# Optimization experiments

Measured on AMD Instinct MI355X. Metric: run time of the kernel, lower is better.

The kernel has to match this reference:

```python
import jax, jax.numpy as jnp
import numpy as np

H, D, VD = 8, 64, 64
QD, KD, VDIM, OUT = 512, 512, 512, 512
N, QS, VS = 16, 512, 512
TEMP = 10.0              # softstair_temp
SCALING = D ** -0.5


def _softstair(x):
    fl = jnp.floor(x)
    return fl + jax.nn.sigmoid(TEMP * (jnp.abs(x - fl) - 0.5))


def setup_inputs() -> dict:
    key = jax.random.key(0)
    ks = jax.random.split(key, 24)
    f = jax.random.normal
    s = 0.03  # xavier-ish scale
    return {
        "Q": f(ks[0], (N, QS, QD), jnp.float32),
        "K": f(ks[1], (N, VS, KD), jnp.float32),
        "V": f(ks[2], (N, VS, VDIM), jnp.float32),
        "past_state": f(ks[3], (N, H, QS, D), jnp.float32),
        "past_attention": jax.random.uniform(ks[4], (N, H, QS, 1), jnp.float32),
        "value_positions": jnp.arange(VS, dtype=jnp.float32),
        "attention_mask": jnp.ones((N, QS, VS), jnp.int32),
        "Wq": f(ks[5], (QD, H * D), jnp.float32) * s,
        "Wk": f(ks[6], (KD, H * D), jnp.float32) * s,
        "Wv": f(ks[7], (VDIM, H * VD), jnp.float32) * s,
        "Wpos": f(ks[8], (QD, H * D), jnp.float32) * s,
        "bpos": f(ks[9], (H * D,), jnp.float32) * s,
        "Wsigma": f(ks[10], (H, D, 1), jnp.float32) * s,
        "Wrho": f(ks[11], (H, D, 3), jnp.float32) * s,
        "mix_w": f(ks[12], (QD, 1), jnp.float32) * s,
        "mix_b": f(ks[13], (1,), jnp.float32) * s,
        "gru_wi": f(ks[14], (D, 3 * D), jnp.float32) * s,
        "gru_wh": f(ks[15], (D, 3 * D), jnp.float32) * s,
        "gru_bi": f(ks[16], (3 * D,), jnp.float32) * s,
        "gru_bh": f(ks[17], (3 * D,), jnp.float32) * s,
        "Wc": f(ks[18], (H * VD, OUT), jnp.float32) * s,
    }


def reference(Q, K, V, past_state, past_attention, value_positions, attention_mask,
              Wq, Wk, Wv, Wpos, bpos, Wsigma, Wrho, mix_w, mix_b,
              gru_wi, gru_wh, gru_bi, gru_bh, Wc):
    n, qS, _ = Q.shape
    vS = K.shape[1]
    mask_f = attention_mask.astype(jnp.float32)          # [N,qS,vS]
    mask_b = attention_mask.astype(bool)[:, None]        # [N,1,qS,vS]
    lengths = jnp.sum(mask_f, axis=-1)                   # [N,qS]
    l_1 = jnp.maximum(1.0, lengths - 1.0)[:, None, :, None]
    step_size = 1.0 / l_1                                # [N,1,qS,1]
    nvp = value_positions[None, None, None, :] * step_size  # [N,1,qS,vS]

    # mix gate
    mix = jax.nn.sigmoid(Q @ mix_w + mix_b)[:, None]     # [N,1,qS,1]

    # projections -> [N,H,S,d]
    Qpos = (Q @ Wpos + bpos).reshape(n, qS, H, D).transpose(0, 2, 1, 3)
    Qh = (Q @ Wq).reshape(n, qS, H, D).transpose(0, 2, 1, 3)
    Kh = (K @ Wk).reshape(n, vS, H, D).transpose(0, 2, 1, 3)
    Vh = (V @ Wv).reshape(n, vS, H, VD).transpose(0, 2, 1, 3)

    # content attention
    content = jnp.einsum('bhqd,bhkd->bhqk', Qh, Kh) * SCALING
    content_attn = jax.nn.softmax(jnp.where(mask_b, content, -jnp.inf), axis=-1)

    # GRUCell update (torch gate order r,z,n) on relu(Qpos) with past_state
    x = jax.nn.relu(Qpos)
    gi = x @ gru_wi + gru_bi
    gh = past_state @ gru_wh + gru_bh
    ir, iz, inn = jnp.split(gi, 3, axis=-1)
    hr, hz, hn = jnp.split(gh, 3, axis=-1)
    r = jax.nn.sigmoid(ir + hr)
    z = jax.nn.sigmoid(iz + hz)
    nn_ = jnp.tanh(inn + r * hn)
    state = (1.0 - z) * nn_ + z * past_state             # [N,H,qS,D]

    # location (Gaussian) attention
    sigma = (jax.nn.relu(jnp.einsum('bhqd,hde->bhqe', state, Wsigma)) + 0.27) \
            / lengths[:, None, :, None]                  # [N,H,qS,1]
    rho = jnp.einsum('bhqd,hde->bhqe', state, Wrho)      # [N,H,qS,3]
    steps = _softstair(rho[..., 0:1])
    attn_gate = jax.nn.sigmoid(rho[..., 1:2])
    bias_gate = jax.nn.sigmoid(rho[..., 2:3])
    mu_ = steps * step_size + attn_gate * past_attention + bias_gate
    # leaky clamp to [0,1]
    mu = jnp.maximum(0.01 * mu_, jnp.minimum(mu_, 1.0 + 0.01 * mu_))
    diff = nvp - mu                                      # [N,H,qS,vS]
    gauss = jnp.exp(-(diff * diff) / (2.0 * sigma * sigma))
    g = gauss * mask_f[:, None]
    pos_attn = g / jnp.sum(g + 1e-20, axis=-1, keepdims=True)

    scores = mix * pos_attn + (1.0 - mix) * content_attn
    attended = jnp.einsum('bhqk,bhkv->bhqv', scores, Vh)
    out = attended.transpose(0, 2, 1, 3).reshape(n, qS, H * VD) @ Wc
    return out
```

## Files before the change

kernel.cpp:

```cpp
#include <hip/hip_runtime.h>


typedef __bf16 bf16;
typedef __bf16 bfx8 __attribute__((ext_vector_type(8)));
typedef float v4f __attribute__((ext_vector_type(4)));

__device__ inline float sigm(float x) { return 1.0f / (1.0f + __expf(-x)); }
__device__ inline float tanh_fast(float x) { return 1.0f - 2.0f / (__expf(2.0f * x) + 1.0f); }

__device__ inline v4f mfma16(bfx8 a, bfx8 b, v4f c) {
    return __builtin_amdgcn_mfma_f32_16x16x32_bf16(a, b, c, 0, 0, 0);
}

typedef const __attribute__((address_space(1))) void* gvp;
typedef __attribute__((address_space(3))) void* lvp;

__device__ inline void gload_lds16(const bf16* g, bf16* l) {
    __builtin_amdgcn_global_load_lds((gvp)g, (lvp)l, 16, 0, 0);
}

__device__ inline void split8(const float* __restrict__ p, bfx8& hi, bfx8& lo) {
    float4 x = *(const float4*)p;
    float4 y = *(const float4*)(p + 4);
    float v[8] = {x.x, x.y, x.z, x.w, y.x, y.y, y.z, y.w};
#pragma unroll
    for (int j = 0; j < 8; ++j) {
        bf16 h = (bf16)v[j];
        hi[j] = h;
        lo[j] = (bf16)(v[j] - (float)h);
    }
}

struct TW { const float* src[5]; bf16* dst[5]; bf16* dstlo[5]; };

__global__ __launch_bounds__(256) void trans_w_kernel(TW a) {
    __shared__ float tile[64][68];
    const float* src = a.src[blockIdx.y];
    bf16* dst = a.dst[blockIdx.y];
    bf16* dlo = a.dstlo[blockIdx.y];
    const int rbase = (blockIdx.x >> 3) * 64, cbase = (blockIdx.x & 7) * 64;
    const int t = threadIdx.x;
    const int r = t >> 2, cc = (t & 3) * 16;
    {
        const float* p = src + (long)(rbase + r) * 512 + cbase + cc;
        *(float4*)(&tile[r][cc]) = *(const float4*)p;
        *(float4*)(&tile[r][cc + 4]) = *(const float4*)(p + 4);
        *(float4*)(&tile[r][cc + 8]) = *(const float4*)(p + 8);
        *(float4*)(&tile[r][cc + 12]) = *(const float4*)(p + 12);
    }
    __syncthreads();
    {
        bfx8 h0, h1, l0, l1;
#pragma unroll
        for (int j = 0; j < 8; ++j) {
            float v0 = tile[cc + j][r];
            float v1 = tile[cc + 8 + j][r];
            bf16 a0 = (bf16)v0, a1 = (bf16)v1;
            h0[j] = a0; l0[j] = (bf16)(v0 - (float)a0);
            h1[j] = a1; l1[j] = (bf16)(v1 - (float)a1);
        }
        const int n_ = cbase + r;
        const int x_ = (n_ & 7) << 3;
        const long rowo = (long)n_ * 512;
        const int ka = (rbase + cc) ^ x_;
        const int kb = (rbase + cc + 8) ^ x_;
        *(bfx8*)(dst + rowo + ka) = h0;
        *(bfx8*)(dst + rowo + kb) = h1;
        if (dlo) {
            *(bfx8*)(dlo + rowo + ka) = l0;
            *(bfx8*)(dlo + rowo + kb) = l1;
        }
    }
}

__global__ void gru_prep_kernel(const float* __restrict__ gwi, const float* __restrict__ gwh,
                                bf16* ih, bf16* il, bf16* hh, bf16* hl) {
    const float* src = blockIdx.x ? gwh : gwi;
    bf16* dh = blockIdx.x ? hh : ih;
    bf16* dl = blockIdx.x ? hl : il;
    int n = threadIdx.x;
    for (int k = 0; k < 64; ++k) {
        float v = src[k * 192 + n];
        bf16 h = (bf16)v;
        dh[n * 64 + k] = h;
        dl[n * 64 + k] = (bf16)(v - (float)h);
    }
}

struct GEMMDesc {
    const float* Af;
    const bf16* Ab;
    const bf16* B0;
    const bf16* B1;
    const float* bias;
    bf16* Cb;
    bf16* Cl;
    float* Cf;
    int mode;
};
struct G4 { GEMMDesc d[4]; };

__global__ __launch_bounds__(256, 4) void gemm128(G4 gg) {
    __shared__ bf16 sm[16384];
    bf16* As = sm;
    bf16* Bs = sm + 8192;

    const GEMMDesc g = gg.d[blockIdx.z];
    const int mode = g.mode;
    const int mbase = blockIdx.x * 128, nbase = blockIdx.y * 128;
    const int t = threadIdx.x, w = t >> 6, l = t & 63;
    const int quad = l >> 4, c = l & 15;
    const int wr = w >> 1, wc = w & 1;

    const v4f zero4 = {0.f, 0.f, 0.f, 0.f};
    v4f acc[4][4];
#pragma unroll
    for (int m = 0; m < 4; ++m)
#pragma unroll
        for (int nn = 0; nn < 4; ++nn) acc[m][nn] = zero4;

    const int nsteps = (mode == 2) ? 24 : 8;
    const int arow_t = t >> 3;
    const int ach = t & 7;
    const int asw = ((ach ^ (arow_t & 7)) * 8);
    const int xm = c & 7;

    for (int s = 0; s < nsteps; ++s) {
        const bf16* Bsrc = g.B0;
        int k0;
        bool lo = false;
        if (mode == 2) {
            int ph = s >> 3;
            k0 = (s & 7) * 64;
            if (ph == 1) Bsrc = g.B1;
            lo = (ph == 2);
        } else {
            k0 = s * 64;
        }

#pragma unroll
        for (int j = 0; j < 4; ++j) {
            int slot = w * 4 + j;
            int row = slot * 8 + (l >> 3);
            const bf16* src = Bsrc + (long)(nbase + row) * 512 + k0 + (l & 7) * 8;
            gload_lds16(src, Bs + slot * 512);
        }
        if (mode == 3) {
#pragma unroll
            for (int j = 0; j < 4; ++j) {
                int slot = w * 4 + j;
                int row = slot * 8 + (l >> 3);
                const bf16* src = g.Ab + (long)(mbase + row) * 512 + k0 + (l & 7) * 8;
                gload_lds16(src, As + slot * 512);
            }
        } else {
#pragma unroll
            for (int j = 0; j < 4; ++j) {
                int row = j * 32 + arow_t;
                const float* p = g.Af + (long)(mbase + row) * 512 + k0 + ach * 8;
                float4 x = *(const float4*)p, y = *(const float4*)(p + 4);
                float v[8] = {x.x, x.y, x.z, x.w, y.x, y.y, y.z, y.w};
                bfx8 hv;
                if (!lo) {
#pragma unroll
                    for (int q = 0; q < 8; ++q) hv[q] = (bf16)v[q];
                } else {
#pragma unroll
                    for (int q = 0; q < 8; ++q) {
                        bf16 h = (bf16)v[q];
                        hv[q] = (bf16)(v[q] - (float)h);
                    }
                }
                *(bfx8*)(&As[row * 64 + asw]) = hv;
            }
        }
        __syncthreads();

#pragma unroll
        for (int ks = 0; ks < 2; ++ks) {
            const int off = (((ks * 4 + quad) ^ xm) * 8);
            bfx8 af[4], bb[4];
#pragma unroll
            for (int m = 0; m < 4; ++m)
                af[m] = *(const bfx8*)(&As[(wr * 64 + m * 16 + c) * 64 + off]);
#pragma unroll
            for (int nn = 0; nn < 4; ++nn)
                bb[nn] = *(const bfx8*)(&Bs[(wc * 64 + nn * 16 + c) * 64 + off]);
#pragma unroll
            for (int m = 0; m < 4; ++m)
#pragma unroll
                for (int nn = 0; nn < 4; ++nn)
                    acc[m][nn] = mfma16(af[m], bb[nn], acc[m][nn]);
        }
        __syncthreads();
    }

    if (mode == 3) {
        float* C = g.Cf;
#pragma unroll
        for (int m = 0; m < 4; ++m)
#pragma unroll
            for (int nn = 0; nn < 4; ++nn)
#pragma unroll
                for (int i = 0; i < 4; ++i) {
                    int row = mbase + wr * 64 + m * 16 + quad * 4 + i;
                    int col = nbase + wc * 64 + nn * 16 + c;
                    C[(long)row * 512 + col] = acc[m][nn][i];
                }
        return;
    }

    if (mode == 1) {
        bf16* CT = g.Cb + ((long)(mbase >> 9)) * 262144;
        const int s0 = mbase & 511;
        for (int h = 0; h < 2; ++h) {
            if (wr == h) {
#pragma unroll
                for (int m = 0; m < 4; ++m)
#pragma unroll
                    for (int nn = 0; nn < 4; ++nn)
#pragma unroll
                        for (int i = 0; i < 4; ++i)
                            sm[(wc * 64 + nn * 16 + c) * 64 + m * 16 + quad * 4 + i] =
                                (bf16)acc[m][nn][i];
            }
            __syncthreads();
            {
                const bf16* src = sm + (t >> 1) * 64 + (t & 1) * 32;
                bf16* d = CT + (long)(nbase + (t >> 1)) * 512 + s0 + h * 64 + (t & 1) * 32;
#pragma unroll
                for (int j = 0; j < 4; ++j) *(bfx8*)(d + j * 8) = *(const bfx8*)(src + j * 8);
            }
            __syncthreads();
        }
        return;
    }

    for (int h = 0; h < 2; ++h) {
        if (wr == h) {
#pragma unroll
            for (int m = 0; m < 4; ++m)
#pragma unroll
                for (int nn = 0; nn < 4; ++nn)
#pragma unroll
                    for (int i = 0; i < 4; ++i) {
                        int col = wc * 64 + nn * 16 + c;
                        float v = acc[m][nn][i];
                        if (mode == 2) v = fmaxf(v + g.bias[nbase + col], 0.f);
                        bf16 hv = (bf16)v;
                        sm[(m * 16 + quad * 4 + i) * 128 + col] = hv;
                        if (mode == 2)
                            sm[8192 + (m * 16 + quad * 4 + i) * 128 + col] =
                                (bf16)(v - (float)hv);
                    }
        }
        __syncthreads();
        {
            const int row = t >> 2, seg = t & 3;
            const bf16* src = sm + row * 128 + seg * 32;
            bf16* d = g.Cb + (long)(mbase + h * 64 + row) * 512 + nbase + seg * 32;
#pragma unroll
            for (int j = 0; j < 4; ++j) *(bfx8*)(d + j * 8) = *(const bfx8*)(src + j * 8);
            if (mode == 2) {
                const bf16* src2 = sm + 8192 + row * 128 + seg * 32;
                bf16* d2 = g.Cl + (long)(mbase + h * 64 + row) * 512 + nbase + seg * 32;
#pragma unroll
                for (int j = 0; j < 4; ++j) *(bfx8*)(d2 + j * 8) = *(const bfx8*)(src2 + j * 8);
            }
        }
        __syncthreads();
    }
}

__global__ __launch_bounds__(256) void mix_len_kernel(
    const float* __restrict__ Q, const int* __restrict__ mask,
    const float* __restrict__ mix_w, const float* __restrict__ mix_b,
    float* __restrict__ mixv, float* __restrict__ stepv, float* __restrict__ lenv,
    unsigned* __restrict__ maskbits) {
    int row = blockIdx.x * 4 + (threadIdx.x >> 6);
    int lane = threadIdx.x & 63;
    float dot = 0.f, ms = 0.f;
    unsigned myw = 0;
#pragma unroll
    for (int j = 0; j < 8; ++j) {
        float qv = Q[(long)row * 512 + j * 64 + lane];
        float wv = mix_w[j * 64 + lane];
        dot += qv * wv;
        int mv = mask[(long)row * 512 + j * 64 + lane];
        unsigned long long b = __ballot(mv != 0);
        ms += (float)__popcll(b);
        if ((lane >> 1) == j) myw = (unsigned)(b >> ((lane & 1) * 32));
    }
#pragma unroll
    for (int o = 32; o > 0; o >>= 1) dot += __shfl_xor(dot, o);
    if (lane < 16) maskbits[(long)row * 16 + lane] = myw;
    if (lane == 0) {
        mixv[row] = sigm(dot + mix_b[0]);
        lenv[row] = ms;
        stepv[row] = 1.0f / fmaxf(1.0f, ms - 1.0f);
    }
}

__global__ __launch_bounds__(256) void gru_fused_kernel(
    const bf16* __restrict__ Xh, const bf16* __restrict__ Xl,
    const float* __restrict__ hp,
    const bf16* __restrict__ wih, const bf16* __restrict__ wil,
    const bf16* __restrict__ whh, const bf16* __restrict__ whl,
    const float* __restrict__ gbi, const float* __restrict__ gbh,
    const float* __restrict__ pa, const float* __restrict__ Wsigma,
    const float* __restrict__ Wrho,
    const float* __restrict__ lenv, const float* __restrict__ stepv,
    float* __restrict__ muv, float* __restrict__ sigv) {
    __shared__ bf16 Wh[192][72], Wl[192][72];
    __shared__ float biL[384];

    const int b = blockIdx.x;
    const int qb = b & 7, nh = b >> 3, hd = nh & 7, n = nh >> 3;
    const int t = threadIdx.x;
    const int w = t >> 6, lane = t & 63, quad = lane >> 4, c = lane & 15;
    const int q0 = qb * 64 + w * 16;

    if (t < 192) { biL[t] = gbi[t]; biL[192 + t] = gbh[t]; }
#pragma unroll
    for (int it = 0; it < 6; ++it) {
        int task = it * 256 + t;
        int r = task >> 3, ch = task & 7;
        *(bfx8*)(&Wh[r][ch * 8]) = *(const bfx8*)(wih + r * 64 + ch * 8);
        *(bfx8*)(&Wl[r][ch * 8]) = *(const bfx8*)(wil + r * 64 + ch * 8);
    }
    __syncthreads();

    const v4f zero4 = {0.f, 0.f, 0.f, 0.f};
    v4f gi[12], gh[12];
#pragma unroll
    for (int nt = 0; nt < 12; ++nt) gi[nt] = zero4;
#pragma unroll
    for (int ks = 0; ks < 2; ++ks) {
        long ao = (long)(n * 512 + q0 + c) * 512 + hd * 64 + ks * 32 + quad * 8;
        bfx8 xh = *(const bfx8*)(Xh + ao);
        bfx8 xl = *(const bfx8*)(Xl + ao);
#pragma unroll
        for (int nt = 0; nt < 12; ++nt) {
            bfx8 bh = *(const bfx8*)(&Wh[nt * 16 + c][ks * 32 + quad * 8]);
            bfx8 bl = *(const bfx8*)(&Wl[nt * 16 + c][ks * 32 + quad * 8]);
            gi[nt] = mfma16(xh, bh, gi[nt]);
            gi[nt] = mfma16(xh, bl, gi[nt]);
            gi[nt] = mfma16(xl, bh, gi[nt]);
        }
    }
    __syncthreads();
#pragma unroll
    for (int it = 0; it < 6; ++it) {
        int task = it * 256 + t;
        int r = task >> 3, ch = task & 7;
        *(bfx8*)(&Wh[r][ch * 8]) = *(const bfx8*)(whh + r * 64 + ch * 8);
        *(bfx8*)(&Wl[r][ch * 8]) = *(const bfx8*)(whl + r * 64 + ch * 8);
    }
    __syncthreads();
#pragma unroll
    for (int nt = 0; nt < 12; ++nt) gh[nt] = zero4;
#pragma unroll
    for (int ks = 0; ks < 2; ++ks) {
        bfx8 ah, al;
        split8(hp + (long)(nh * 512 + q0 + c) * 64 + ks * 32 + quad * 8, ah, al);
#pragma unroll
        for (int nt = 0; nt < 12; ++nt) {
            bfx8 bh = *(const bfx8*)(&Wh[nt * 16 + c][ks * 32 + quad * 8]);
            bfx8 bl = *(const bfx8*)(&Wl[nt * 16 + c][ks * 32 + quad * 8]);
            gh[nt] = mfma16(ah, bh, gh[nt]);
            gh[nt] = mfma16(ah, bl, gh[nt]);
            gh[nt] = mfma16(al, bh, gh[nt]);
        }
    }

    float st[4][4];
#pragma unroll
    for (int t4 = 0; t4 < 4; ++t4) {
        float bir = biL[t4 * 16 + c];
        float biz = biL[64 + t4 * 16 + c];
        float bin = biL[128 + t4 * 16 + c];
        float bhr = biL[192 + t4 * 16 + c];
        float bhz = biL[256 + t4 * 16 + c];
        float bhn = biL[320 + t4 * 16 + c];
#pragma unroll
        for (int i = 0; i < 4; ++i) {
            int row = q0 + quad * 4 + i;
            float r = sigm(gi[t4][i] + bir + gh[t4][i] + bhr);
            float z = sigm(gi[t4 + 4][i] + biz + gh[t4 + 4][i] + bhz);
            float nn_ = tanh_fast(gi[t4 + 8][i] + bin + r * (gh[t4 + 8][i] + bhn));
            float hpv = hp[(long)(nh * 512 + row) * 64 + t4 * 16 + c];
            st[t4][i] = (1.0f - z) * nn_ + z * hpv;
        }
    }

    float ws_[4], wr0[4], wr1[4], wr2[4];
#pragma unroll
    for (int t4 = 0; t4 < 4; ++t4) {
        int d = t4 * 16 + c;
        ws_[t4] = Wsigma[hd * 64 + d];
        wr0[t4] = Wrho[(hd * 64 + d) * 3 + 0];
        wr1[t4] = Wrho[(hd * 64 + d) * 3 + 1];
        wr2[t4] = Wrho[(hd * 64 + d) * 3 + 2];
    }
#pragma unroll
    for (int i = 0; i < 4; ++i) {
        float s0 = 0.f, s1 = 0.f, s2 = 0.f, s3 = 0.f;
#pragma unroll
        for (int t4 = 0; t4 < 4; ++t4) {
            float sv = st[t4][i];
            s0 += sv * ws_[t4];
            s1 += sv * wr0[t4];
            s2 += sv * wr1[t4];
            s3 += sv * wr2[t4];
        }
#pragma unroll
        for (int o = 1; o < 16; o <<= 1) {
            s0 += __shfl_xor(s0, o);
            s1 += __shfl_xor(s1, o);
            s2 += __shfl_xor(s2, o);
            s3 += __shfl_xor(s3, o);
        }
        if (c == 0) {
            int row = q0 + quad * 4 + i;
            int idx = nh * 512 + row, rq = n * 512 + row;
            float L = lenv[rq], sp = stepv[rq];
            float sg = (fmaxf(s0, 0.f) + 0.27f) / L;
            float fl = floorf(s1);
            float steps = fl + sigm(10.0f * (fabsf(s1 - fl) - 0.5f));
            float ag = sigm(s2), bg = sigm(s3);
            float mu_ = steps * sp + ag * pa[idx] + bg;
            float mu = fmaxf(0.01f * mu_, fminf(mu_, 1.0f + 0.01f * mu_));
            muv[idx] = mu;
            sigv[idx] = sg;
        }
    }
}

__global__ __launch_bounds__(256) void attn_fused_kernel(
    const bf16* __restrict__ Qh, const bf16* __restrict__ Kh,
    const bf16* __restrict__ VhT, const unsigned* __restrict__ maskbits,
    const float* __restrict__ vpos, const float* __restrict__ mixv,
    const float* __restrict__ stepv, const float* __restrict__ muv,
    const float* __restrict__ sigv, bf16* __restrict__ att) {
    __shared__ bf16 Pp[16][520];
    __shared__ bf16 Pg[16][520];
    __shared__ float rsum[4][16], rgsum[4][16];

    const int b = blockIdx.x;
    const int nh = ((b >> 8) << 3) | (b & 7);
    const int qt = (b >> 3) & 31;
    const int hd = nh & 7, n = nh >> 3;
    const int t = threadIdx.x;
    const int wave = t >> 6, lane = t & 63;
    const int quad = lane >> 4, c = lane & 15;
    const int qloc = quad * 4;

    const bf16* qrow = Qh + (long)(n * 512 + qt * 16 + c) * 512 + hd * 64 + quad * 8;
    bfx8 afr0 = *(const bfx8*)qrow;
    bfx8 afr1 = *(const bfx8*)(qrow + 32);

    const v4f zero4 = {0.f, 0.f, 0.f, 0.f};
    v4f acc[8];
#pragma unroll
    for (int i = 0; i < 8; ++i) acc[i] = zero4;

    const bf16* kbase = Kh + (long)(n * 512 + wave * 128 + c) * 512 + hd * 64 + quad * 8;
#pragma unroll
    for (int t8 = 0; t8 < 8; ++t8) {
        bfx8 b0 = *(const bfx8*)(kbase + (long)t8 * 16 * 512);
        bfx8 b1 = *(const bfx8*)(kbase + (long)t8 * 16 * 512 + 32);
        acc[t8] = mfma16(afr0, b0, acc[t8]);
        acc[t8] = mfma16(afr1, b1, acc[t8]);
    }

    float mu_[4], i2s[4], stp[4];
#pragma unroll
    for (int i = 0; i < 4; ++i) {
        int q = qt * 16 + qloc + i;
        int idx = nh * 512 + q, rq = n * 512 + q;
        mu_[i] = muv[idx];
        float sg = sigv[idx];
        i2s[i] = 0.5f / (sg * sg);
        stp[i] = stepv[rq];
    }

    unsigned mbits[4];
    {
        const unsigned* mrow = maskbits + ((long)(n * 512 + qt * 16) << 4) + wave * 4;
#pragma unroll
        for (int i = 0; i < 4; ++i) {
            const unsigned* mr = mrow + ((qloc + i) << 4);
            unsigned w0 = mr[0], w1 = mr[1], w2 = mr[2], w3 = mr[3];
            mbits[i] = ((w0 >> c) & 1u) | (((w0 >> (16 + c)) & 1u) << 1) |
                       (((w1 >> c) & 1u) << 2) | (((w1 >> (16 + c)) & 1u) << 3) |
                       (((w2 >> c) & 1u) << 4) | (((w2 >> (16 + c)) & 1u) << 5) |
                       (((w3 >> c) & 1u) << 6) | (((w3 >> (16 + c)) & 1u) << 7);
        }
    }

    float vp[8];
#pragma unroll
    for (int t8 = 0; t8 < 8; ++t8) vp[t8] = vpos[wave * 128 + t8 * 16 + c];

    float psum[4] = {0.f, 0.f, 0.f, 0.f};
    float gsum[4] = {0.f, 0.f, 0.f, 0.f};
#pragma unroll
    for (int i = 0; i < 4; ++i) {
        float m = mu_[i], s = stp[i], c2 = i2s[i];
#pragma unroll
        for (int t8 = 0; t8 < 8; ++t8) {
            int on = (mbits[i] >> t8) & 1;
            float pv = on ? __expf(acc[t8][i] * 0.125f) : 0.f;
            float d = vp[t8] * s - m;
            float gv = on ? __expf(-(d * d) * c2) : 0.f;
            psum[i] += pv;
            gsum[i] += gv;
            int k = wave * 128 + t8 * 16 + c;
            Pp[qloc + i][k] = (bf16)pv;
            Pg[qloc + i][k] = (bf16)gv;
        }
    }
#pragma unroll
    for (int i = 0; i < 4; ++i) {
#pragma unroll
        for (int o = 1; o < 16; o <<= 1) {
            psum[i] += __shfl_xor(psum[i], o);
            gsum[i] += __shfl_xor(gsum[i], o);
        }
        if (c == 0) {
            rsum[wave][qloc + i] = psum[i];
            rgsum[wave][qloc + i] = gsum[i];
        }
    }

    __syncthreads();

    float ac[4], bc[4];
#pragma unroll
    for (int i = 0; i < 4; ++i) {
        float Sp = rsum[0][qloc + i] + rsum[1][qloc + i] + rsum[2][qloc + i] + rsum[3][qloc + i];
        float Sg = rgsum[0][qloc + i] + rgsum[1][qloc + i] + rgsum[2][qloc + i] +
                   rgsum[3][qloc + i] + 512.0f * 1e-20f;
        float m_ = mixv[n * 512 + qt * 16 + qloc + i];
        ac[i] = (1.0f - m_) / Sp;
        bc[i] = m_ / Sg;
    }

    v4f accP = zero4, accG = zero4;
    const bf16* vrow = VhT + (long)(n * 512 + hd * 64 + wave * 16 + c) * 512 + quad * 8;
#pragma unroll
    for (int ks = 0; ks < 16; ++ks) {
        bfx8 bf_ = *(const bfx8*)(vrow + ks * 32);
        bfx8 ap = *(const bfx8*)(&Pp[c][ks * 32 + quad * 8]);
        bfx8 ag = *(const bfx8*)(&Pg[c][ks * 32 + quad * 8]);
        accP = mfma16(ap, bf_, accP);
        accG = mfma16(ag, bf_, accG);
    }

#pragma unroll
    for (int i = 0; i < 4; ++i) {
        int q = qt * 16 + quad * 4 + i;
        int cx = (wave * 16 + c) ^ (((quad * 4 + i) & 7) << 3);
        att[(long)(n * 512 + q) * 512 + hd * 64 + cx] =
            (bf16)(ac[i] * accP[i] + bc[i] * accG[i]);
    }
}

extern "C" void kernel_launch(void* const* d_in, const int* in_sizes, int n_in,
                              void* d_out, int out_size, void* d_ws, size_t ws_size,
                              hipStream_t stream) {
    (void)in_sizes; (void)n_in; (void)out_size; (void)ws_size;

    const float* Q = (const float*)d_in[0];
    const float* K = (const float*)d_in[1];
    const float* V = (const float*)d_in[2];
    const float* past_state = (const float*)d_in[3];
    const float* past_att = (const float*)d_in[4];
    const float* vpos = (const float*)d_in[5];
    const int* mask = (const int*)d_in[6];
    const float* Wq = (const float*)d_in[7];
    const float* Wk = (const float*)d_in[8];
    const float* Wv = (const float*)d_in[9];
    const float* Wpos = (const float*)d_in[10];
    const float* bpos = (const float*)d_in[11];
    const float* Wsigma = (const float*)d_in[12];
    const float* Wrho = (const float*)d_in[13];
    const float* mix_w = (const float*)d_in[14];
    const float* mix_b = (const float*)d_in[15];
    const float* gwi = (const float*)d_in[16];
    const float* gwh = (const float*)d_in[17];
    const float* gbi = (const float*)d_in[18];
    const float* gbh = (const float*)d_in[19];
    const float* Wc = (const float*)d_in[20];
    float* out = (float*)d_out;

    char* p = (char*)d_ws;
    const size_t SZB = 8192UL * 512 * 2;
    const size_t SZW = 512UL * 512 * 2;
    bf16* WqT = (bf16*)p;   p += SZW;
    bf16* WkT = (bf16*)p;   p += SZW;
    bf16* WvT = (bf16*)p;   p += SZW;
    bf16* WpT = (bf16*)p;   p += SZW;
    bf16* WpTl = (bf16*)p;  p += SZW;
    bf16* WcT = (bf16*)p;   p += SZW;
    bf16* wih = (bf16*)p;   p += 24576;
    bf16* wil = (bf16*)p;   p += 24576;
    bf16* whh = (bf16*)p;   p += 24576;
    bf16* whl = (bf16*)p;   p += 24576;
    bf16* Qh = (bf16*)p;    p += SZB;
    bf16* Kh = (bf16*)p;    p += SZB;
    bf16* VhT = (bf16*)p;   p += SZB;
    bf16* Xh = (bf16*)p;
    bf16* att = Xh;         p += SZB;
    bf16* Xl = (bf16*)p;    p += SZB;
    unsigned* maskbits = (unsigned*)p;   p += 8192UL * 16 * 4;
    float* mixv = (float*)p;  p += 32768;
    float* stepv = (float*)p; p += 32768;
    float* lenv = (float*)p;  p += 32768;
    float* muv = (float*)p;   p += 262144;
    float* sigv = (float*)p;  p += 262144;

    dim3 blk(256);

    TW tw;
    tw.src[0] = Wq; tw.src[1] = Wk; tw.src[2] = Wv; tw.src[3] = Wpos; tw.src[4] = Wc;
    tw.dst[0] = WqT; tw.dst[1] = WkT; tw.dst[2] = WvT; tw.dst[3] = WpT; tw.dst[4] = WcT;
    tw.dstlo[0] = nullptr; tw.dstlo[1] = nullptr; tw.dstlo[2] = nullptr;
    tw.dstlo[3] = WpTl; tw.dstlo[4] = nullptr;
    trans_w_kernel<<<dim3(64, 5), blk, 0, stream>>>(tw);

    gru_prep_kernel<<<dim3(2), dim3(192), 0, stream>>>(gwi, gwh, wih, wil, whh, whl);

    mix_len_kernel<<<dim3(2048), blk, 0, stream>>>(Q, mask, mix_w, mix_b, mixv, stepv, lenv, maskbits);

    G4 gp;
    gp.d[0].Af = Q;  gp.d[0].Ab = nullptr; gp.d[0].B0 = WpT; gp.d[0].B1 = WpTl;
    gp.d[0].bias = bpos; gp.d[0].Cb = Xh; gp.d[0].Cl = Xl; gp.d[0].Cf = nullptr; gp.d[0].mode = 2;
    gp.d[1].Af = Q;  gp.d[1].Ab = nullptr; gp.d[1].B0 = WqT; gp.d[1].B1 = nullptr;
    gp.d[1].bias = nullptr; gp.d[1].Cb = Qh; gp.d[1].Cl = nullptr; gp.d[1].Cf = nullptr; gp.d[1].mode = 0;
    gp.d[2].Af = K;  gp.d[2].Ab = nullptr; gp.d[2].B0 = WkT; gp.d[2].B1 = nullptr;
    gp.d[2].bias = nullptr; gp.d[2].Cb = Kh; gp.d[2].Cl = nullptr; gp.d[2].Cf = nullptr; gp.d[2].mode = 0;
    gp.d[3].Af = V;  gp.d[3].Ab = nullptr; gp.d[3].B0 = WvT; gp.d[3].B1 = nullptr;
    gp.d[3].bias = nullptr; gp.d[3].Cb = VhT; gp.d[3].Cl = nullptr; gp.d[3].Cf = nullptr; gp.d[3].mode = 1;
    gemm128<<<dim3(64, 4, 4), blk, 0, stream>>>(gp);

    gru_fused_kernel<<<dim3(1024), blk, 0, stream>>>(
        Xh, Xl, past_state, wih, wil, whh, whl, gbi, gbh, past_att, Wsigma, Wrho,
        lenv, stepv, muv, sigv);

    attn_fused_kernel<<<dim3(4096), blk, 0, stream>>>(
        Qh, Kh, VhT, maskbits, vpos, mixv, stepv, muv, sigv, att);

    G4 go;
    go.d[0].Af = nullptr; go.d[0].Ab = att; go.d[0].B0 = WcT; go.d[0].B1 = nullptr;
    go.d[0].bias = nullptr; go.d[0].Cb = nullptr; go.d[0].Cl = nullptr; go.d[0].Cf = out;
    go.d[0].mode = 3;
    go.d[1] = go.d[0]; go.d[2] = go.d[0]; go.d[3] = go.d[0];
    gemm128<<<dim3(64, 4, 1), blk, 0, stream>>>(go);
}
```

Baseline: 370.7 us.

## Double-buffer GEMM LDS tiles to overlap global loads with MFMA compute

Converts the gemm128 main loop into a two-stage software pipeline with double-buffered shared memory. The next K-step's B tile (and A for mode 3) is issued asynchronously to LDS, and the next A tile's fp32 values are loaded into registers, all before computing on the current buffer. Those A values are converted and stored afterwards, and one barrier per step replaces two. Shared memory doubles to 64KB and launch bounds drop to 2 blocks per CU, which lowers occupancy and adds register pressure.

```diff
diff --git a/kernel.cpp b/kernel.cpp
--- a/kernel.cpp
+++ b/kernel.cpp
@@ -100,10 +100,8 @@
 };
 struct G4 { GEMMDesc d[4]; };
 
-__global__ __launch_bounds__(256, 4) void gemm128(G4 gg) {
-    __shared__ bf16 sm[16384];
-    bf16* As = sm;
-    bf16* Bs = sm + 8192;
+__global__ __launch_bounds__(256, 2) void gemm128(G4 gg) {
+    __shared__ bf16 sm[32768];
 
     const GEMMDesc g = gg.d[blockIdx.z];
     const int mode = g.mode;
@@ -124,58 +122,68 @@
     const int ach = t & 7;
     const int asw = ((ach ^ (arow_t & 7)) * 8);
     const int xm = c & 7;
-
-    for (int s = 0; s < nsteps; ++s) {
+    const int slot0 = w * 4;
+    const int srow = l >> 3;
+    const int sch8 = (l & 7) * 8;
+
+    float4 ax[4], ay[4];
+
+    auto issue = [&](int s, bf16* As, bf16* Bs) {
         const bf16* Bsrc = g.B0;
         int k0;
-        bool lo = false;
         if (mode == 2) {
             int ph = s >> 3;
             k0 = (s & 7) * 64;
             if (ph == 1) Bsrc = g.B1;
-            lo = (ph == 2);
         } else {
             k0 = s * 64;
         }
-
 #pragma unroll
         for (int j = 0; j < 4; ++j) {
-            int slot = w * 4 + j;
-            int row = slot * 8 + (l >> 3);
-            const bf16* src = Bsrc + (long)(nbase + row) * 512 + k0 + (l & 7) * 8;
-            gload_lds16(src, Bs + slot * 512);
+            int sl = slot0 + j;
+            int row = sl * 8 + srow;
+            gload_lds16(Bsrc + (long)(nbase + row) * 512 + k0 + sch8, Bs + sl * 512);
         }
         if (mode == 3) {
 #pragma unroll
             for (int j = 0; j < 4; ++j) {
-                int slot = w * 4 + j;
-                int row = slot * 8 + (l >> 3);
-                const bf16* src = g.Ab + (long)(mbase + row) * 512 + k0 + (l & 7) * 8;
-                gload_lds16(src, As + slot * 512);
+                int sl = slot0 + j;
+                int row = sl * 8 + srow;
+                gload_lds16(g.Ab + (long)(mbase + row) * 512 + k0 + sch8, As + sl * 512);
             }
         } else {
 #pragma unroll
             for (int j = 0; j < 4; ++j) {
-                int row = j * 32 + arow_t;
-                const float* p = g.Af + (long)(mbase + row) * 512 + k0 + ach * 8;
-                float4 x = *(const float4*)p, y = *(const float4*)(p + 4);
-                float v[8] = {x.x, x.y, x.z, x.w, y.x, y.y, y.z, y.w};
-                bfx8 hv;
-                if (!lo) {
-#pragma unroll
-                    for (int q = 0; q < 8; ++q) hv[q] = (bf16)v[q];
-                } else {
-#pragma unroll
-                    for (int q = 0; q < 8; ++q) {
-                        bf16 h = (bf16)v[q];
-                        hv[q] = (bf16)(v[q] - (float)h);
-                    }
+                const float* p = g.Af + (long)(mbase + j * 32 + arow_t) * 512 + k0 + ach * 8;
+                ax[j] = *(const float4*)p;
+                ay[j] = *(const float4*)(p + 4);
+            }
+        }
+    };
+
+    auto writeA = [&](int s, bf16* As) {
+        if (mode == 3) return;
+        const bool lo = (mode == 2) && ((s >> 3) == 2);
+#pragma unroll
+        for (int j = 0; j < 4; ++j) {
+            float v[8] = {ax[j].x, ax[j].y, ax[j].z, ax[j].w,
+                          ay[j].x, ay[j].y, ay[j].z, ay[j].w};
+            bfx8 hv;
+            if (!lo) {
+#pragma unroll
+                for (int q = 0; q < 8; ++q) hv[q] = (bf16)v[q];
+            } else {
+#pragma unroll
+                for (int q = 0; q < 8; ++q) {
+                    bf16 h = (bf16)v[q];
+                    hv[q] = (bf16)(v[q] - (float)h);
                 }
-                *(bfx8*)(&As[row * 64 + asw]) = hv;
             }
-        }
-        __syncthreads();
-
+            *(bfx8*)(&As[(j * 32 + arow_t) * 64 + asw]) = hv;
+        }
+    };
+
+    auto compute = [&](const bf16* As, const bf16* Bs) {
 #pragma unroll
         for (int ks = 0; ks < 2; ++ks) {
             const int off = (((ks * 4 + quad) ^ xm) * 8);
@@ -192,6 +200,18 @@
                 for (int nn = 0; nn < 4; ++nn)
                     acc[m][nn] = mfma16(af[m], bb[nn], acc[m][nn]);
         }
+    };
+
+    issue(0, sm, sm + 8192);
+    writeA(0, sm);
+    __syncthreads();
+    for (int s = 0; s < nsteps; ++s) {
+        bf16* Ac = sm + (s & 1) * 16384;
+        bf16* An = sm + (((s & 1) ^ 1) * 16384);
+        const bool more = (s + 1 < nsteps);
+        if (more) issue(s + 1, An, An + 8192);
+        compute(Ac, Ac + 8192);
+        if (more) writeA(s + 1, An);
         __syncthreads();
     }
 
```

New measurement: 338.1 us. -8.8%, faster.
